# Optimization experiments

Measured on AMD Instinct MI355X. Metric: run time of the kernel, lower is better.

The kernel has to match this reference:

```python
import jax, jax.numpy as jnp
import numpy as np

B, T, C, L = 256, 1024, 128, 64
BLANK = C - 1          # tf.compat.v1.nn.ctc_loss uses num_classes-1 as blank
EPS = 1e-7             # keras.backend.epsilon()
NEG = -1e30            # log-space 'zero'
S = 2 * L + 1          # extended label length (blanks interleaved)


def setup_inputs() -> dict:
    key = jax.random.key(0)
    k1, k2 = jax.random.split(key)
    # y_pred are softmax probabilities (the layer takes log(y_pred + eps))
    y_pred = jax.nn.softmax(jax.random.normal(k1, (B, T, C), dtype=jnp.float32), axis=-1)
    # labels in [0, C-2]; blank (C-1) never appears in targets
    y_true = jax.random.randint(k2, (B, L), 0, C - 1, dtype=jnp.int32)
    return {"y_true": y_true, "y_pred": y_pred}


def _ctc_loss(y_true, y_pred):
    logp = jnp.log(y_pred + EPS)                                   # [B,T,C]
    # extended label sequence: blank, l1, blank, l2, ..., blank -> [B,S]
    ext = jnp.full((B, S), BLANK, dtype=jnp.int32).at[:, 1::2].set(y_true)
    # gather per-extended-symbol log-probs: lp_ext[b,t,s] = logp[b,t,ext[b,s]]
    lp_ext = jnp.take_along_axis(logp[:, :, None, :], ext[:, None, :, None], axis=-1)[..., 0]  # [B,T,S]
    lp_ext = jnp.transpose(lp_ext, (1, 0, 2))                      # [T,B,S] time-major for scan
    # skip transition allowed where ext[s] != blank and ext[s] != ext[s-2]
    can_skip = jnp.concatenate(
        [jnp.zeros((B, 2), dtype=bool), (ext[:, 2:] != BLANK) & (ext[:, 2:] != ext[:, :-2])],
        axis=1)                                                    # [B,S]

    def shift(a, n):
        return jnp.concatenate([jnp.full((B, n), NEG, a.dtype), a[:, : S - n]], axis=1)

    # alpha init at t=0: only s=0 (blank) and s=1 (first label) reachable
    alpha0 = (jnp.full((B, S), NEG)
              .at[:, 0].set(lp_ext[0, :, 0])
              .at[:, 1].set(lp_ext[0, :, 1]))

    def step(alpha, lp_t):
        s1 = shift(alpha, 1)
        s2 = jnp.where(can_skip, shift(alpha, 2), NEG)
        m = jnp.maximum(alpha, jnp.maximum(s1, s2))                # stable log-sum-exp of 3 terms
        new = m + jnp.log(jnp.exp(alpha - m) + jnp.exp(s1 - m) + jnp.exp(s2 - m)) + lp_t
        return new, None

    alphaT, _ = jax.lax.scan(step, alpha0, lp_ext[1:])
    log_lik = jnp.logaddexp(alphaT[:, -1], alphaT[:, -2])          # end in last blank or last label
    return (-log_lik)[:, None]                                     # [B,1], matches expand_dims(..., 1)


def reference(y_true, y_pred):
    return _ctc_loss(y_true, y_pred)
```

## Files before the change

kernel.cpp:

```cpp
#include <hip/hip_runtime.h>


#define B_     256
#define T_     1024
#define C_     128
#define L_     64
#define BLANK_ 127
#define LN2_   0.69314718055994530942f
#define ROWS   32
#define LDSF   (ROWS * C_)

__device__ __forceinline__ float flog2(float x) { return __builtin_amdgcn_logf(x); }

template <int CTRL>
__device__ __forceinline__ int dpp_i(int x) {
    return __builtin_amdgcn_update_dpp(x, x, CTRL, 0xF, 0xF, false);
}
__device__ __forceinline__ float ror1_f(float x) {
    return __int_as_float(dpp_i<0x13C>(__float_as_int(x)));
}
__device__ __forceinline__ int ror1_i(int x) { return dpp_i<0x13C>(x); }

__device__ __forceinline__ float fldexp(float x, int n) {
#if __has_builtin(__builtin_amdgcn_ldexpf)
    return __builtin_amdgcn_ldexpf(x, n);
#else
    return ldexpf(x, n);
#endif
}
__device__ __forceinline__ int fexp_of(float x) {
#if __has_builtin(__builtin_amdgcn_frexp_expf)
    return __builtin_amdgcn_frexp_expf(x);
#else
    const int bx = (__float_as_int(x) >> 23) & 0xFF;
    return (x > 0.0f) ? (bx - 126) : 0;
#endif
}

typedef const __attribute__((address_space(1))) void gas_void;
typedef __attribute__((address_space(3))) void las_void;
__device__ __forceinline__ void g2l16(const float* g, float* l) {
    __builtin_amdgcn_global_load_lds((gas_void*)g, (las_void*)l, 16, 0, 0);
}
__device__ __forceinline__ void g2l4(const float* g, float* l) {
    __builtin_amdgcn_global_load_lds((gas_void*)g, (las_void*)l, 4, 0, 0);
}

#define ALSTEP(pL, pB)                                                        \
    {                                                                         \
        const int   ep  = ror1_i(e);                                          \
        const float mpO = ror1_f(aO);                                         \
        const bool dead = (fmaxf(aE, aO) == 0.0f);                            \
        e = dead ? ep : e;                                                    \
        const int   dd  = ep - e;                                             \
        float prevO = fldexp(mpO, dd);                                        \
        prevO = isL0 ? 0.0f : prevO;                                          \
        const float sk = can_skip ? prevO : 0.0f;                             \
        const float nE = (aE + prevO) * (pB);                                 \
        const float nO = (aO + aE + sk) * (pL);                               \
        aZ = (aZ + aO) * (pB);                                                \
        aE = nE; aO = nO;                                                     \
    }

#define RENORM4                                                               \
    {                                                                         \
        const int x = fexp_of(fmaxf(aE, aO));                                 \
        aE = fldexp(aE, -x); aO = fldexp(aO, -x); aZ = fldexp(aZ, -x);        \
        e += x;                                                               \
    }

#define DCALC                                                                 \
    {                                                                         \
        const int ep = ror1_i(e);                                             \
        d = isL0 ? (-16384) : (ep - e);                                       \
    }

#define RENORM4B { RENORM4 DCALC }

#define BLSTEP(pL, pB)                                                        \
    {                                                                         \
        const float prevO = fldexp(ror1_f(aO), d);                            \
        const float nE = (aE + prevO) * (pB);                                 \
        const float nO = __builtin_fmaf(skf, prevO, aO + aE) * (pL);          \
        aZ = (aZ + aO) * (pB);                                                \
        aE = nE; aO = nO;                                                     \
    }

#define ACHUNK(RL, RB)                                                        \
    {                                                                         \
        _Pragma("unroll")                                                     \
        for (int k = 0; k < 32; ++k) {                                        \
            ALSTEP(RL[k], RB[k])                                              \
            if ((k & 3) == 3) RENORM4                                         \
        }                                                                     \
    }

#define BCHUNK32(RL, RB)                                                      \
    {                                                                         \
        _Pragma("unroll")                                                     \
        for (int k = 0; k < 32; ++k) {                                        \
            BLSTEP(RL[k], RB[k])                                              \
            if ((k & 3) == 3) RENORM4B                                        \
        }                                                                     \
    }

#define STAGE_CHUNK(k, LOFF)                                                  \
    {                                                                         \
        const float* src = base + (size_t)(1 + 32 * (k)) * C_;                \
        const int nKB = ((k) == 31) ? 15 : 16;                                \
        _Pragma("unroll")                                                     \
        for (int j = 0; j < 16; ++j)                                          \
            if (j < nKB)                                                      \
                g2l16(src + j * 256 + lane * 4, sm + (LOFF) + j * 256);       \
        if ((k) == 31) {                                                      \
            const float* s2 = src + 15 * 256;                                 \
            g2l4(s2 + lane,      sm + (LOFF) + 15 * 256);                     \
            g2l4(s2 + 64 + lane, sm + (LOFF) + 15 * 256 + 64);                \
        }                                                                     \
    }

#define BURST(LOFF, RL, RB, NR)                                               \
    {                                                                         \
        const float* pl = &sm[(LOFF) + lab];                                  \
        const float* pb = &sm[(LOFF) + BLANK_];                               \
        _Pragma("unroll")                                                     \
        for (int j = 0; j < (NR); ++j) RL[j] = pl[j * C_];                    \
        _Pragma("unroll")                                                     \
        for (int j = 0; j < (NR); ++j) RB[j] = pb[j * C_];                    \
    }

#define VMWAIT asm volatile("s_waitcnt vmcnt(0)" ::: "memory")

__global__ __launch_bounds__(64, 1)
void ctc_fwd(const int* __restrict__ yt, const float* __restrict__ yp,
             float* __restrict__ out) {
    __shared__ float sm[3 * LDSF];

    const int b    = blockIdx.x;
    const int lane = threadIdx.x;
    const int lab  = yt[b * L_ + lane];
    const int labp = __shfl_up(lab, 1);
    const bool can_skip = (lane > 0) && (lab != labp);
    const bool isL0     = (lane == 0);
    const float skf     = can_skip ? 1.0f : 0.0f;

    const float* __restrict__ base = yp + (size_t)b * T_ * C_;

    STAGE_CHUNK(0, 0)
    STAGE_CHUNK(1, LDSF)

    float aE = isL0 ? base[BLANK_] : 0.0f;
    float aO = isL0 ? base[lab]    : 0.0f;
    float aZ = 0.0f;
    int   e  = 0, d = 0;

    VMWAIT;

    float rl0[32], rb0[32], rl1[32], rb1[32];
    BURST(0, rl0, rb0, 32)

    STAGE_CHUNK(2, 2 * LDSF)
    BURST(LDSF, rl1, rb1, 32)
    ACHUNK(rl0, rb0)
    VMWAIT;

    STAGE_CHUNK(3, 0)
    BURST(2 * LDSF, rl0, rb0, 32)
    ACHUNK(rl1, rb1)
    VMWAIT;

    STAGE_CHUNK(4, LDSF)
    BURST(0, rl1, rb1, 32)
    ACHUNK(rl0, rb0)
    VMWAIT;

    STAGE_CHUNK(5, 2 * LDSF)
    BURST(LDSF, rl0, rb0, 32)
    ACHUNK(rl1, rb1)
    VMWAIT;

    DCALC

#pragma unroll 1
    for (int c = 4; c <= 28; c += 2) {
        {
            STAGE_CHUNK(c + 2, ((c + 2) % 3) * LDSF)
            BURST(((c + 1) % 3) * LDSF, rl1, rb1, 32)
            BCHUNK32(rl0, rb0)
            VMWAIT;
        }
        {
            STAGE_CHUNK(c + 3, ((c + 3) % 3) * LDSF)
            BURST(((c + 2) % 3) * LDSF, rl0, rb0, 32)
            BCHUNK32(rl1, rb1)
            VMWAIT;
        }
    }

    BURST((31 % 3) * LDSF, rl1, rb1, 31)
    BCHUNK32(rl0, rb0)

#pragma unroll
    for (int k = 0; k < 31; ++k) {
        BLSTEP(rl1[k], rb1[k])
        if ((k & 3) == 3) RENORM4B
    }

    if (lane == 63) {
        const float s = aO + aZ;
        out[b] = -(flog2(s) + (float)e) * LN2_;
    }
}

extern "C" void kernel_launch(void* const* d_in, const int* in_sizes, int n_in,
                              void* d_out, int out_size, void* d_ws, size_t ws_size,
                              hipStream_t stream) {
    const int*   y_true = (const int*)d_in[0];
    const float* y_pred = (const float*)d_in[1];
    float*       out    = (float*)d_out;
    ctc_fwd<<<B_, 64, 0, stream>>>(y_true, y_pred, out);
}
```

Baseline: 198.3 us.

## Split CTC recursion into concurrent forward and backward halves meeting at midpoint

The kernel now launches two wavefronts per batch item. One runs the alpha forward recursion over the first half of time steps and the other runs a beta backward recursion over the second half, each with its own triple-buffered LDS staging. The two partial results are combined through shared memory with a scaled-exponent dot product and a wave reduction. This aims to halve the serial dependency chain length, at the cost of doubling LDS use, adding a second recursion implementation, and introducing a midpoint combine with extra numerical bookkeeping.

```diff
diff --git a/kernel.cpp b/kernel.cpp
--- a/kernel.cpp
+++ b/kernel.cpp
@@ -9,6 +9,7 @@
 #define LN2_   0.69314718055994530942f
 #define ROWS   32
 #define LDSF   (ROWS * C_)
+#define XOFF   (6 * LDSF)
 
 __device__ __forceinline__ float flog2(float x) { return __builtin_amdgcn_logf(x); }
 
@@ -20,6 +21,10 @@
     return __int_as_float(dpp_i<0x13C>(__float_as_int(x)));
 }
 __device__ __forceinline__ int ror1_i(int x) { return dpp_i<0x13C>(x); }
+__device__ __forceinline__ float rol1_f(float x) {
+    return __int_as_float(dpp_i<0x134>(__float_as_int(x)));
+}
+__device__ __forceinline__ int rol1_i(int x) { return dpp_i<0x134>(x); }
 
 __device__ __forceinline__ float fldexp(float x, int n) {
 #if __has_builtin(__builtin_amdgcn_ldexpf)
@@ -104,15 +109,15 @@
         }                                                                     \
     }
 
-#define STAGE_CHUNK(k, LOFF)                                                  \
+#define FSTAGE(k, LOFF)                                                       \
     {                                                                         \
         const float* src = base + (size_t)(1 + 32 * (k)) * C_;                \
-        const int nKB = ((k) == 31) ? 15 : 16;                                \
+        const int nKB = ((k) == 15) ? 15 : 16;                                \
         _Pragma("unroll")                                                     \
         for (int j = 0; j < 16; ++j)                                          \
             if (j < nKB)                                                      \
                 g2l16(src + j * 256 + lane * 4, sm + (LOFF) + j * 256);       \
-        if ((k) == 31) {                                                      \
+        if ((k) == 15) {                                                      \
             const float* s2 = src + 15 * 256;                                 \
             g2l4(s2 + lane,      sm + (LOFF) + 15 * 256);                     \
             g2l4(s2 + 64 + lane, sm + (LOFF) + 15 * 256 + 64);                \
@@ -129,86 +134,241 @@
         for (int j = 0; j < (NR); ++j) RB[j] = pb[j * C_];                    \
     }
 
+#define ABSTEP(pL, pB)                                                        \
+    {                                                                         \
+        const float u  = bO * (pL);                                           \
+        const float v  = bE * (pB);                                           \
+        const int   eR = rol1_i(eb);                                          \
+        const float mU = rol1_f(u);                                           \
+        const float mV = rol1_f(v);                                           \
+        const bool dead = (fmaxf(bE, bO) == 0.0f);                            \
+        eb = dead ? eR : eb;                                                  \
+        const int   dd = eR - eb;                                             \
+        const float bZn = bZ * (pB);                                          \
+        float w  = fldexp(mV, dd);                                            \
+        float x2 = fldexp(mU, dd);                                            \
+        w  = isL63 ? bZn : w;                                                 \
+        x2 = isL63 ? 0.0f : x2;                                               \
+        bE = v + u;                                                           \
+        bO = __builtin_fmaf(sknf, x2, u + w);                                 \
+        bZ = bZn;                                                             \
+    }
+
+#define BRENORM4                                                              \
+    {                                                                         \
+        const int x = fexp_of(fmaxf(bE, bO));                                 \
+        bE = fldexp(bE, -x); bO = fldexp(bO, -x); bZ = fldexp(bZ, -x);        \
+        eb += x;                                                              \
+    }
+
+#define DBCALC                                                                \
+    {                                                                         \
+        const int eR = rol1_i(eb);                                            \
+        dB = isL63 ? (-16384) : (eR - eb);                                    \
+    }
+
+#define BRENORM4B { BRENORM4 DBCALC }
+
+#define BLSTEPB(pL, pB)                                                       \
+    {                                                                         \
+        const float u  = bO * (pL);                                           \
+        const float v  = bE * (pB);                                           \
+        const float bZn = bZ * (pB);                                          \
+        float w  = fldexp(rol1_f(v), dB);                    \
+        const float x2 = fldexp(rol1_f(u), dB);                               \
+        w = isL63 ? bZn : w;                                                  \
+        bE = v + u;                                                           \
+        bO = __builtin_fmaf(sknf, x2, u + w);                                 \
+        bZ = bZn;                                                             \
+    }
+
+#define ABCHUNK(RL, RB)                                                       \
+    {                                                                         \
+        _Pragma("unroll")                                                     \
+        for (int k = 0; k < 32; ++k) {                                        \
+            ABSTEP(RL[k], RB[k])                                              \
+            if ((k & 3) == 3) BRENORM4                                        \
+        }                                                                     \
+    }
+
+#define BBCHUNK32(RL, RB)                                                     \
+    {                                                                         \
+        _Pragma("unroll")                                                     \
+        for (int k = 0; k < 32; ++k) {                                        \
+            BLSTEPB(RL[k], RB[k])                                             \
+            if ((k & 3) == 3) BRENORM4B                                       \
+        }                                                                     \
+    }
+
+#define BSTAGE(m, LOFF)                                                       \
+    {                                                                         \
+        const float* src = base + (size_t)(992 - 32 * (m)) * C_;              \
+        _Pragma("unroll")                                                     \
+        for (int j = 0; j < 16; ++j)                                          \
+            g2l16(src + j * 256 + lane * 4, sm + (LOFF) + j * 256);           \
+    }
+
+#define BBURST(LOFF, RL, RB)                                                  \
+    {                                                                         \
+        const float* pl = &sm[(LOFF) + lab];                                  \
+        const float* pb = &sm[(LOFF) + BLANK_];                               \
+        _Pragma("unroll")                                                     \
+        for (int j = 0; j < 32; ++j) RL[j] = pl[(31 - j) * C_];               \
+        _Pragma("unroll")                                                     \
+        for (int j = 0; j < 32; ++j) RB[j] = pb[(31 - j) * C_];               \
+    }
+
 #define VMWAIT asm volatile("s_waitcnt vmcnt(0)" ::: "memory")
 
-__global__ __launch_bounds__(64, 1)
+__global__ __launch_bounds__(128, 1)
 void ctc_fwd(const int* __restrict__ yt, const float* __restrict__ yp,
              float* __restrict__ out) {
-    __shared__ float sm[3 * LDSF];
+    __shared__ float sm[6 * LDSF + 256];
 
     const int b    = blockIdx.x;
-    const int lane = threadIdx.x;
+    const int tid  = threadIdx.x;
+    const int wid  = tid >> 6;
+    const int lane = tid & 63;
     const int lab  = yt[b * L_ + lane];
     const int labp = __shfl_up(lab, 1);
     const bool can_skip = (lane > 0) && (lab != labp);
     const bool isL0     = (lane == 0);
+    const bool isL63    = (lane == 63);
     const float skf     = can_skip ? 1.0f : 0.0f;
+    const float sknf    = rol1_f(skf);
 
     const float* __restrict__ base = yp + (size_t)b * T_ * C_;
 
-    STAGE_CHUNK(0, 0)
-    STAGE_CHUNK(1, LDSF)
-
-    float aE = isL0 ? base[BLANK_] : 0.0f;
-    float aO = isL0 ? base[lab]    : 0.0f;
-    float aZ = 0.0f;
-    int   e  = 0, d = 0;
-
-    VMWAIT;
-
-    float rl0[32], rb0[32], rl1[32], rb1[32];
-    BURST(0, rl0, rb0, 32)
-
-    STAGE_CHUNK(2, 2 * LDSF)
-    BURST(LDSF, rl1, rb1, 32)
-    ACHUNK(rl0, rb0)
-    VMWAIT;
-
-    STAGE_CHUNK(3, 0)
-    BURST(2 * LDSF, rl0, rb0, 32)
-    ACHUNK(rl1, rb1)
-    VMWAIT;
-
-    STAGE_CHUNK(4, LDSF)
-    BURST(0, rl1, rb1, 32)
-    ACHUNK(rl0, rb0)
-    VMWAIT;
-
-    STAGE_CHUNK(5, 2 * LDSF)
-    BURST(LDSF, rl0, rb0, 32)
-    ACHUNK(rl1, rb1)
-    VMWAIT;
-
-    DCALC
-
+    float aE = 0.0f, aO = 0.0f, aZ = 0.0f;
+    int   e  = 0;
+
+    if (wid == 0) {
+        int d = 0;
+        FSTAGE(0, 0)
+        FSTAGE(1, LDSF)
+        aE = isL0 ? base[BLANK_] : 0.0f;
+        aO = isL0 ? base[lab]    : 0.0f;
+        VMWAIT;
+
+        float rl0[32], rb0[32], rl1[32], rb1[32];
+        BURST(0, rl0, rb0, 32)
+
+        FSTAGE(2, 2 * LDSF)
+        BURST(LDSF, rl1, rb1, 32)
+        ACHUNK(rl0, rb0)
+        VMWAIT;
+        FSTAGE(3, 0)
+        BURST(2 * LDSF, rl0, rb0, 32)
+        ACHUNK(rl1, rb1)
+        VMWAIT;
+        FSTAGE(4, LDSF)
+        BURST(0, rl1, rb1, 32)
+        ACHUNK(rl0, rb0)
+        VMWAIT;
+        FSTAGE(5, 2 * LDSF)
+        BURST(LDSF, rl0, rb0, 32)
+        ACHUNK(rl1, rb1)
+        VMWAIT;
+
+        DCALC
 #pragma unroll 1
-    for (int c = 4; c <= 28; c += 2) {
-        {
-            STAGE_CHUNK(c + 2, ((c + 2) % 3) * LDSF)
-            BURST(((c + 1) % 3) * LDSF, rl1, rb1, 32)
-            BCHUNK32(rl0, rb0)
-            VMWAIT;
+        for (int c = 4; c <= 12; c += 2) {
+            {
+                FSTAGE(c + 2, ((c + 2) % 3) * LDSF)
+                BURST(((c + 1) % 3) * LDSF, rl1, rb1, 32)
+                BCHUNK32(rl0, rb0)
+                VMWAIT;
+            }
+            {
+                FSTAGE(c + 3, ((c + 3) % 3) * LDSF)
+                BURST(((c + 2) % 3) * LDSF, rl0, rb0, 32)
+                BCHUNK32(rl1, rb1)
+                VMWAIT;
+            }
         }
-        {
-            STAGE_CHUNK(c + 3, ((c + 3) % 3) * LDSF)
-            BURST(((c + 2) % 3) * LDSF, rl0, rb0, 32)
-            BCHUNK32(rl1, rb1)
-            VMWAIT;
+        BURST(0, rl1, rb1, 31)
+        BCHUNK32(rl0, rb0)
+#pragma unroll
+        for (int k = 0; k < 31; ++k) {
+            BLSTEP(rl1[k], rb1[k])
+            if ((k & 3) == 3) RENORM4B
         }
-    }
-
-    BURST((31 % 3) * LDSF, rl1, rb1, 31)
-    BCHUNK32(rl0, rb0)
-
+    } else {
+        int eb = 0, dB = 0;
+        float bE = 0.0f;
+        float bO = isL63 ? 1.0f : 0.0f;
+        float bZ = isL63 ? 1.0f : 0.0f;
+
+        BSTAGE(0, 3 * LDSF)
+        BSTAGE(1, 4 * LDSF)
+        VMWAIT;
+
+        float rl0[32], rb0[32], rl1[32], rb1[32];
+        BBURST(3 * LDSF, rl0, rb0)
+
+        BSTAGE(2, 5 * LDSF)
+        BBURST(4 * LDSF, rl1, rb1)
+        ABCHUNK(rl0, rb0)
+        VMWAIT;
+        BSTAGE(3, 3 * LDSF)
+        BBURST(5 * LDSF, rl0, rb0)
+        ABCHUNK(rl1, rb1)
+        VMWAIT;
+        BSTAGE(4, 4 * LDSF)
+        BBURST(3 * LDSF, rl1, rb1)
+        ABCHUNK(rl0, rb0)
+        VMWAIT;
+        BSTAGE(5, 5 * LDSF)
+        BBURST(4 * LDSF, rl0, rb0)
+        ABCHUNK(rl1, rb1)
+        VMWAIT;
+
+        DBCALC
+#pragma unroll 1
+        for (int m = 4; m <= 12; m += 2) {
+            {
+                BSTAGE(m + 2, (3 + (m + 2) % 3) * LDSF)
+                BBURST((3 + (m + 1) % 3) * LDSF, rl1, rb1)
+                BBCHUNK32(rl0, rb0)
+                VMWAIT;
+            }
+            {
+                BSTAGE(m + 3, (3 + (m + 3) % 3) * LDSF)
+                BBURST((3 + (m + 2) % 3) * LDSF, rl0, rb0)
+                BBCHUNK32(rl1, rb1)
+                VMWAIT;
+            }
+        }
+        BBURST(3 * LDSF, rl1, rb1)
+        BBCHUNK32(rl0, rb0)
+        BBCHUNK32(rl1, rb1)
+
+        sm[XOFF + lane]       = bE;
+        sm[XOFF + 64 + lane]  = bO;
+        sm[XOFF + 128 + lane] = __int_as_float(eb);
+        sm[XOFF + 192 + lane] = bZ;
+    }
+
+    __syncthreads();
+
+    if (wid == 0) {
+        const float bE2 = sm[XOFF + lane];
+        const float bO2 = sm[XOFF + 64 + lane];
+        const int   eb2 = __float_as_int(sm[XOFF + 128 + lane]);
+        const float bZ2 = sm[XOFF + 192 + lane];
+        float s = aE * bE2 + aO * bO2;
+        if (isL63) s = __builtin_fmaf(aZ, bZ2, s);
+        int E = e + eb2;
+        E = (s == 0.0f) ? (int)0xE0000000 : E;
 #pragma unroll
-    for (int k = 0; k < 31; ++k) {
-        BLSTEP(rl1[k], rb1[k])
-        if ((k & 3) == 3) RENORM4B
-    }
-
-    if (lane == 63) {
-        const float s = aO + aZ;
-        out[b] = -(flog2(s) + (float)e) * LN2_;
+        for (int off = 1; off < 64; off <<= 1) {
+            const float s2 = __shfl_xor(s, off);
+            const int   E2 = __shfl_xor(E, off);
+            const int   Em = (E > E2) ? E : E2;
+            s = fldexp(s, E - Em) + fldexp(s2, E2 - Em);
+            E = Em;
+        }
+        if (tid == 0) out[b] = -(flog2(s) + (float)E) * LN2_;
     }
 }
 
@@ -218,5 +378,5 @@
     const int*   y_true = (const int*)d_in[0];
     const float* y_pred = (const float*)d_in[1];
     float*       out    = (float*)d_out;
-    ctc_fwd<<<B_, 64, 0, stream>>>(y_true, y_pred, out);
-}
+    ctc_fwd<<<B_, 128, 0, stream>>>(y_true, y_pred, out);
+}
```

Result: no change. 195.9 us (-1.2%).

## Split CTC recursion into forward and backward halves meeting at midpoint

Applied to the files above, without the earlier changes.

Each block now runs two wavefronts: one computes the alpha recursion forward over the first half of time steps, the other computes a beta-style recursion backward from the end over the second half. The two meet at the midpoint through LDS, and wave 0 combines them with an exponent-tracked reduction across lanes. This roughly halves the serial dependency chain per batch element, which bounds latency at one wave per block. The cost is a second wave per block, double the LDS staging, and a more delicate combine step at the boundary, where an indexing or scaling mistake would give wrong results.

```diff
diff --git a/kernel.cpp b/kernel.cpp
--- a/kernel.cpp
+++ b/kernel.cpp
@@ -9,6 +9,7 @@
 #define LN2_   0.69314718055994530942f
 #define ROWS   32
 #define LDSF   (ROWS * C_)
+#define XOFF   (6 * LDSF)
 
 __device__ __forceinline__ float flog2(float x) { return __builtin_amdgcn_logf(x); }
 
@@ -41,9 +42,6 @@
 typedef __attribute__((address_space(3))) void las_void;
 __device__ __forceinline__ void g2l16(const float* g, float* l) {
     __builtin_amdgcn_global_load_lds((gas_void*)g, (las_void*)l, 16, 0, 0);
-}
-__device__ __forceinline__ void g2l4(const float* g, float* l) {
-    __builtin_amdgcn_global_load_lds((gas_void*)g, (las_void*)l, 4, 0, 0);
 }
 
 #define ALSTEP(pL, pB)                                                        \
@@ -104,111 +102,158 @@
         }                                                                     \
     }
 
-#define STAGE_CHUNK(k, LOFF)                                                  \
-    {                                                                         \
-        const float* src = base + (size_t)(1 + 32 * (k)) * C_;                \
-        const int nKB = ((k) == 31) ? 15 : 16;                                \
+#define STAGE16(ROW, LOFF)                                                    \
+    {                                                                         \
+        const float* src = base + (size_t)(ROW) * C_;                         \
         _Pragma("unroll")                                                     \
         for (int j = 0; j < 16; ++j)                                          \
-            if (j < nKB)                                                      \
-                g2l16(src + j * 256 + lane * 4, sm + (LOFF) + j * 256);       \
-        if ((k) == 31) {                                                      \
-            const float* s2 = src + 15 * 256;                                 \
-            g2l4(s2 + lane,      sm + (LOFF) + 15 * 256);                     \
-            g2l4(s2 + 64 + lane, sm + (LOFF) + 15 * 256 + 64);                \
-        }                                                                     \
-    }
-
-#define BURST(LOFF, RL, RB, NR)                                               \
+            g2l16(src + j * 256 + lane * 4, sm + (LOFF) + j * 256);           \
+    }
+
+#define FBURSTM(LOFF, RL, RB)                                                 \
     {                                                                         \
         const float* pl = &sm[(LOFF) + lab];                                  \
         const float* pb = &sm[(LOFF) + BLANK_];                               \
         _Pragma("unroll")                                                     \
-        for (int j = 0; j < (NR); ++j) RL[j] = pl[j * C_];                    \
-        _Pragma("unroll")                                                     \
-        for (int j = 0; j < (NR); ++j) RB[j] = pb[j * C_];                    \
+        for (int j = 0; j < 32; ++j) RL[j] = pl[j * C_];                      \
+        _Pragma("unroll")                                                     \
+        for (int j = 0; j < 32; ++j) RB[j] = pb[j * C_];                      \
+    }
+#define RBURSTM(LOFF, RL, RB)                                                 \
+    {                                                                         \
+        const float* pl = &sm[(LOFF) + lab];                                  \
+        const float* pb = &sm[(LOFF) + BLANK_];                               \
+        _Pragma("unroll")                                                     \
+        for (int j = 0; j < 32; ++j) RL[j] = pl[(31 - j) * C_];               \
+        _Pragma("unroll")                                                     \
+        for (int j = 0; j < 32; ++j) RB[j] = pb[(31 - j) * C_];               \
     }
 
 #define VMWAIT asm volatile("s_waitcnt vmcnt(0)" ::: "memory")
 
-__global__ __launch_bounds__(64, 1)
+#define RUN_HALF(SB, CHUNKROW, BURSTM)                                        \
+    {                                                                         \
+        float rl0[32], rb0[32], rl1[32], rb1[32];                             \
+        STAGE16(CHUNKROW(0), (SB))                                            \
+        STAGE16(CHUNKROW(1), (SB) + LDSF)                                     \
+        aE = isL0 ? ibase[BLANK_] : 0.0f;                                     \
+        aO = isL0 ? ibase[lab]    : 0.0f;                                     \
+        VMWAIT;                                                               \
+        BURSTM((SB), rl0, rb0)                                   \
+        STAGE16(CHUNKROW(2), (SB) + 2 * LDSF)                                 \
+        BURSTM((SB) + LDSF, rl1, rb1)                            \
+        ACHUNK(rl0, rb0)                                                      \
+        VMWAIT;                                                               \
+        STAGE16(CHUNKROW(3), (SB))                                            \
+        BURSTM((SB) + 2 * LDSF, rl0, rb0)                        \
+        ACHUNK(rl1, rb1)                                                      \
+        VMWAIT;                                                               \
+        STAGE16(CHUNKROW(4), (SB) + LDSF)                                     \
+        BURSTM((SB), rl1, rb1)                                   \
+        ACHUNK(rl0, rb0)                                                      \
+        VMWAIT;                                                               \
+        STAGE16(CHUNKROW(5), (SB) + 2 * LDSF)                                 \
+        BURSTM((SB) + LDSF, rl0, rb0)                            \
+        ACHUNK(rl1, rb1)                                                      \
+        VMWAIT;                                                               \
+        DCALC                                                                 \
+        _Pragma("unroll 1")                                                   \
+        for (int c = 4; c <= 12; c += 2) {                                    \
+            STAGE16(CHUNKROW(c + 2), (SB) + ((c + 2) % 3) * LDSF)             \
+            BURSTM((SB) + ((c + 1) % 3) * LDSF, rl1, rb1)                     \
+            BCHUNK32(rl0, rb0)                                                \
+            VMWAIT;                                                           \
+            STAGE16(CHUNKROW(c + 3), (SB) + ((c + 3) % 3) * LDSF)             \
+            BURSTM((SB) + ((c + 2) % 3) * LDSF, rl0, rb0)                     \
+            BCHUNK32(rl1, rb1)                                                \
+            VMWAIT;                                                           \
+        }                                                                     \
+        BURSTM((SB), rl1, rb1)                          \
+        BCHUNK32(rl0, rb0)                                      \
+        _Pragma("unroll")                                                     \
+        for (int k = 0; k < 31; ++k) {                \
+            BLSTEP(rl1[k], rb1[k])                                            \
+            if ((k & 3) == 3) RENORM4B                                        \
+        }                                                                     \
+    }
+
+#define FROW(k) (1 + 32 * (k))
+#define RROW(k) (991 - 32 * (k))
+
+#define ACCP(t, Et)                                                           \
+    {                                                                         \
+        const float t_ = (t); const int Et_ = (Et);                           \
+        const int Em = (Eacc > Et_) ? Eacc : Et_;                             \
+        acc = fldexp(acc, Eacc - Em) + fldexp(t_, Et_ - Em);                  \
+        Eacc = Em;                                                            \
+    }
+
+__global__ __launch_bounds__(128, 1)
 void ctc_fwd(const int* __restrict__ yt, const float* __restrict__ yp,
              float* __restrict__ out) {
-    __shared__ float sm[3 * LDSF];
+    __shared__ float sm[6 * LDSF + 320];
 
     const int b    = blockIdx.x;
-    const int lane = threadIdx.x;
-    const int lab  = yt[b * L_ + lane];
+    const int tid  = threadIdx.x;
+    const int wid  = tid >> 6;
+    const int lane = tid & 63;
+    const int lidx = (wid == 0) ? lane : (63 - lane);
+    const int lab  = yt[b * L_ + lidx];
     const int labp = __shfl_up(lab, 1);
     const bool can_skip = (lane > 0) && (lab != labp);
     const bool isL0     = (lane == 0);
+    const bool isL63    = (lane == 63);
     const float skf     = can_skip ? 1.0f : 0.0f;
 
-    const float* __restrict__ base = yp + (size_t)b * T_ * C_;
-
-    STAGE_CHUNK(0, 0)
-    STAGE_CHUNK(1, LDSF)
-
-    float aE = isL0 ? base[BLANK_] : 0.0f;
-    float aO = isL0 ? base[lab]    : 0.0f;
-    float aZ = 0.0f;
+    const float* __restrict__ base  = yp + (size_t)b * T_ * C_;
+    const float* __restrict__ ibase = (wid == 0) ? base : (base + 1023 * C_);
+
+    float aE = 0.0f, aO = 0.0f, aZ = 0.0f;
     int   e  = 0, d = 0;
 
-    VMWAIT;
-
-    float rl0[32], rb0[32], rl1[32], rb1[32];
-    BURST(0, rl0, rb0, 32)
-
-    STAGE_CHUNK(2, 2 * LDSF)
-    BURST(LDSF, rl1, rb1, 32)
-    ACHUNK(rl0, rb0)
-    VMWAIT;
-
-    STAGE_CHUNK(3, 0)
-    BURST(2 * LDSF, rl0, rb0, 32)
-    ACHUNK(rl1, rb1)
-    VMWAIT;
-
-    STAGE_CHUNK(4, LDSF)
-    BURST(0, rl1, rb1, 32)
-    ACHUNK(rl0, rb0)
-    VMWAIT;
-
-    STAGE_CHUNK(5, 2 * LDSF)
-    BURST(LDSF, rl0, rb0, 32)
-    ACHUNK(rl1, rb1)
-    VMWAIT;
-
-    DCALC
-
-#pragma unroll 1
-    for (int c = 4; c <= 28; c += 2) {
-        {
-            STAGE_CHUNK(c + 2, ((c + 2) % 3) * LDSF)
-            BURST(((c + 1) % 3) * LDSF, rl1, rb1, 32)
-            BCHUNK32(rl0, rb0)
-            VMWAIT;
+    if (wid == 0) {
+        RUN_HALF(0, FROW, FBURSTM)
+    } else {
+        RUN_HALF(3 * LDSF, RROW, RBURSTM)
+        sm[XOFF + lane]        = aE;
+        sm[XOFF + 64 + lane]   = aO;
+        sm[XOFF + 128 + lane]  = __int_as_float(e);
+        sm[XOFF + 192 + lane]  = aZ;
+    }
+
+    __syncthreads();
+
+    if (wid == 0) {
+        const int i = lane;
+        const float rE_hi = isL0 ? sm[XOFF + 192 + 63] : sm[XOFF + 64 - i];
+        const int   e_hi  = __float_as_int(isL0 ? sm[XOFF + 128 + 63]
+                                                : sm[XOFF + 128 + 64 - i]);
+        const float rO_hi = sm[XOFF + 64 + 63 - i];
+        const int   eo_hi = __float_as_int(sm[XOFF + 128 + 63 - i]);
+        const float rE_nx = isL63 ? sm[XOFF] : sm[XOFF + 63 - i];
+        const int   e_nx  = __float_as_int(isL63 ? sm[XOFF + 128]
+                                                 : sm[XOFF + 128 + 63 - i]);
+        const float rO_nx = isL63 ? 0.0f : sm[XOFF + 64 + 62 - i];
+        const int   eo_nx = isL63 ? 0 : __float_as_int(sm[XOFF + 128 + 62 - i]);
+        const int   labn  = __shfl_down(lab, 1);
+        const float sknE  = (!isL63 && labn != lab) ? 1.0f : 0.0f;
+
+        float acc = aE * rE_hi;
+        int  Eacc = e + e_hi;
+        ACCP((aE + aO) * rO_hi, e + eo_hi)
+        ACCP((isL63 ? (aO + aZ) : aO) * rE_nx, e + e_nx)
+        ACCP(sknE * (aO * rO_nx), e + eo_nx)
+        if (acc == 0.0f) Eacc = -(1 << 29);
+
+#pragma unroll
+        for (int off = 1; off < 64; off <<= 1) {
+            const float s2 = __shfl_xor(acc, off);
+            const int   E2 = __shfl_xor(Eacc, off);
+            const int   Em = (Eacc > E2) ? Eacc : E2;
+            acc = fldexp(acc, Eacc - Em) + fldexp(s2, E2 - Em);
+            Eacc = Em;
         }
-        {
-            STAGE_CHUNK(c + 3, ((c + 3) % 3) * LDSF)
-            BURST(((c + 2) % 3) * LDSF, rl0, rb0, 32)
-            BCHUNK32(rl1, rb1)
-            VMWAIT;
-        }
-    }
-
-    BURST((31 % 3) * LDSF, rl1, rb1, 31)
-    BCHUNK32(rl0, rb0)
-
-#pragma unroll
-    for (int k = 0; k < 31; ++k) {
-        BLSTEP(rl1[k], rb1[k])
-        if ((k & 3) == 3) RENORM4B
-    }
-
-    if (lane == 63) {
-        const float s = aO + aZ;
-        out[b] = -(flog2(s) + (float)e) * LN2_;
+        if (tid == 0) out[b] = -(flog2(acc) + (float)Eacc) * LN2_;
     }
 }
 
@@ -218,5 +263,5 @@
     const int*   y_true = (const int*)d_in[0];
     const float* y_pred = (const float*)d_in[1];
     float*       out    = (float*)d_out;
-    ctc_fwd<<<B_, 64, 0, stream>>>(y_true, y_pred, out);
-}
+    ctc_fwd<<<B_, 128, 0, stream>>>(y_true, y_pred, out);
+}
```

Result: no change. 195.5 us (-1.4%).
